# Kernel tuning notes

Measured on AMD Instinct MI355X. Metric: run time of the kernel, lower is better.

## Reference

```python
import jax, jax.numpy as jnp
import numpy as np

L, H = 6, 8          # depth, heads
DM, DH, M = 512, 64, 256  # d_model, d_head, nb random features
EPS = 1e-4


def sinusoidal_pe(n, d, dtype):
    pos = jnp.arange(n, dtype=jnp.float32)[:, None]
    div = jnp.exp(jnp.arange(0, d, 2, dtype=jnp.float32) * (-(np.log(10000.0) / d)))
    pe = jnp.zeros((n, d), jnp.float32)
    pe = pe.at[:, 0::2].set(jnp.sin(pos * div))
    pe = pe.at[:, 1::2].set(jnp.cos(pos * div))
    return pe.astype(dtype)


def layer_norm(x, g, b, eps=1e-5):
    mu = jnp.mean(x, -1, keepdims=True)
    var = jnp.mean(jnp.square(x - mu), -1, keepdims=True)
    return (x - mu) * jax.lax.rsqrt(var + eps) * g + b


def softmax_features(x, proj, is_query):
    # FAVOR+ positive softmax-kernel features. x: [b,h,n,dh], proj: [m,dh]
    dn = DH ** -0.25
    xd = x * dn
    u = jnp.einsum('bhnd,md->bhnm', xd, proj)            # [b,h,n,m]
    diag = 0.5 * jnp.sum(xd * xd, -1, keepdims=True)      # ||x||^2/2 (normalized)
    if is_query:
        stab = jnp.max(u, axis=-1, keepdims=True)
    else:
        stab = jnp.max(u, axis=(-2, -1), keepdims=True)
    return (M ** -0.5) * (jnp.exp(u - diag - stab) + EPS)


def split_heads(t, b, n):
    return t.reshape(b, n, H, DH).transpose(0, 2, 1, 3)   # [b,h,n,dh]


def reference(x, proj, ln1_g, ln1_b, wq, wk, wv, wo, bo, ln2_g, ln2_b, w1, b1, w2, b2):
    b, n, d = x.shape
    x = x + sinusoidal_pe(n, d, x.dtype)[None]
    for i in range(L):
        # --- FAVOR+ linear attention (pre-norm) ---
        h = layer_norm(x, ln1_g[i], ln1_b[i])
        q = split_heads(h @ wq[i], b, n)
        k = split_heads(h @ wk[i], b, n)
        v = split_heads(h @ wv[i], b, n)
        qp = softmax_features(q, proj[i], True)           # [b,h,n,m]
        kp = softmax_features(k, proj[i], False)
        ksum = jnp.sum(kp, axis=2)                         # [b,h,m]
        d_inv = 1.0 / jnp.einsum('bhnm,bhm->bhn', qp, ksum)
        ctx = jnp.einsum('bhnm,bhnd->bhmd', kp, v)         # [b,h,m,dh]
        o = jnp.einsum('bhnm,bhmd->bhnd', qp, ctx) * d_inv[..., None]
        o = o.transpose(0, 2, 1, 3).reshape(b, n, DM)
        x = x + o @ wo[i] + bo[i]
        # --- feed-forward (pre-norm, GELU) ---
        h = layer_norm(x, ln2_g[i], ln2_b[i])
        x = x + jax.nn.gelu(h @ w1[i] + b1[i], approximate=False) @ w2[i] + b2[i]
    return x


def setup_inputs() -> dict:
    key = jax.random.key(0)
    ks = jax.random.split(key, 9)
    s_in = DM ** -0.5
    s_ff = (4 * DM) ** -0.5
    return {
        'x':     jax.random.normal(ks[0], (8, 2048, DM), jnp.float32),
        'proj':  jax.random.normal(ks[1], (L, M, DH), jnp.float32),
        'ln1_g': jnp.ones((L, DM), jnp.float32),
        'ln1_b': jnp.zeros((L, DM), jnp.float32),
        'wq':    jax.random.normal(ks[2], (L, DM, DM), jnp.float32) * s_in,
        'wk':    jax.random.normal(ks[3], (L, DM, DM), jnp.float32) * s_in,
        'wv':    jax.random.normal(ks[4], (L, DM, DM), jnp.float32) * s_in,
        'wo':    jax.random.normal(ks[5], (L, DM, DM), jnp.float32) * s_in,
        'bo':    jnp.zeros((L, DM), jnp.float32),
        'ln2_g': jnp.ones((L, DM), jnp.float32),
        'ln2_b': jnp.zeros((L, DM), jnp.float32),
        'w1':    jax.random.normal(ks[6], (L, DM, 4 * DM), jnp.float32) * s_in,
        'b1':    jnp.zeros((L, 4 * DM), jnp.float32),
        'w2':    jax.random.normal(ks[7], (L, 4 * DM, DM), jnp.float32) * s_ff,
        'b2':    jnp.zeros((L, DM), jnp.float32),
    }
```

## Files before the change

kernel.cpp:

```cpp
#include <hip/hip_runtime.h>
#include <math.h>

#define LNUM 6
#define HNUM 8
#define DMODEL 512
#define DHEAD 64
#define MFEAT 256
#define BATCH 8
#define SEQ 2048
#define TOK (BATCH*SEQ)
#define BHN (BATCH*HNUM)
#define DFF 2048
#define EPSF 1e-4f
#define LN_EPS 1e-5f
#define DNRM 0.35355339059327373f
#define SMF 0.0625f

typedef unsigned short u16;
typedef __attribute__((ext_vector_type(8))) short bf16x8;
typedef __attribute__((ext_vector_type(4))) float f32x4;
#define MFMA16(a,b,c) __builtin_amdgcn_mfma_f32_16x16x32_bf16(a,b,c,0,0,0)

#define GLOAD16(g,l) __builtin_amdgcn_global_load_lds( \
    (const __attribute__((address_space(1))) void*)(g), \
    (__attribute__((address_space(3))) void*)(l), 16, 0, 0)

__device__ __forceinline__ u16 f2bf(float f){
  unsigned int u = __float_as_uint(f);
  u = (u + 0x7fffu + ((u >> 16) & 1u)) >> 16;
  return (u16)u;
}
__device__ __forceinline__ float bf2f(u16 s){
  return __uint_as_float(((unsigned int)s) << 16);
}
__device__ __forceinline__ void atomicMaxF(float* addr, float val){
  if(val >= 0.f) atomicMax((int*)addr, __float_as_int(val));
  else           atomicMin((unsigned int*)addr, __float_as_uint(val));
}
__device__ __forceinline__ float fast_gelu(float z){
  float g2 = z*(1.5957691216f + 0.07135481628f*z*z);
  return z / (1.0f + __expf(-g2));
}

__global__ void k_addpe(const float* __restrict__ x, float* __restrict__ xo){
  int idx = blockIdx.x*256 + threadIdx.x;
  int d = idx & (DMODEL-1);
  int n = (idx >> 9) & (SEQ-1);
  int j = d >> 1;
  float freq = expf((float)(2*j) * (-9.210340371976184f / (float)DMODEL));
  float ang = (float)n * freq;
  float pe = (d & 1) ? cosf(ang) : sinf(ang);
  xo[idx] = x[idx] + pe;
}

__global__ void k_ln(const float* __restrict__ x, const float* __restrict__ g,
                     const float* __restrict__ bv, u16* __restrict__ out){
  __shared__ float sred[8];
  int t = blockIdx.x, tid = threadIdx.x;
  const float2 v = ((const float2*)(x + (size_t)t*DMODEL))[tid];
  float s = v.x + v.y;
  #pragma unroll
  for(int o=32;o;o>>=1) s += __shfl_down(s,o);
  if((tid&63)==0) sred[tid>>6] = s;
  __syncthreads();
  if(tid==0) sred[4] = (sred[0]+sred[1]+sred[2]+sred[3]) * (1.0f/DMODEL);
  __syncthreads();
  float mu = sred[4];
  float dx = v.x - mu, dy = v.y - mu;
  float s2 = dx*dx + dy*dy;
  #pragma unroll
  for(int o=32;o;o>>=1) s2 += __shfl_down(s2,o);
  if((tid&63)==0) sred[tid>>6] = s2;
  __syncthreads();
  if(tid==0) sred[5] = rsqrtf((sred[0]+sred[1]+sred[2]+sred[3])*(1.0f/DMODEL) + LN_EPS);
  __syncthreads();
  float rs = sred[5];
  const float2 gg = ((const float2*)g)[tid];
  const float2 bb = ((const float2*)bv)[tid];
  ushort2 o2; o2.x = f2bf(dx*rs*gg.x + bb.x); o2.y = f2bf(dy*rs*gg.y + bb.y);
  ((ushort2*)(out + (size_t)t*DMODEL))[tid] = o2;
}

__global__ void k_wcvt(const float* __restrict__ w, u16* __restrict__ wt, int K, int N){
  __shared__ float sm[64][65];
  int kt = blockIdx.y*64, nt = blockIdx.x*64;
  int t = threadIdx.x;
  int c = t & 63, r4 = t >> 6;
  #pragma unroll
  for(int i=0;i<16;i++){
    int kl = i*4 + r4;
    sm[kl][c] = w[(size_t)(kt+kl)*N + nt + c];
  }
  __syncthreads();
  #pragma unroll
  for(int i=0;i<16;i++){
    int nl = i*4 + r4;
    wt[(size_t)(nt+nl)*K + kt + c] = f2bf(sm[c][nl]);
  }
}

__global__ void k_pcvt(const float* __restrict__ p, u16* __restrict__ pb){
  int i = blockIdx.x*256 + threadIdx.x;
  pb[i] = f2bf(p[i]);
}

template<int EPI>
__global__ __launch_bounds__(256,4)
void k_mm(const u16* __restrict__ A, const u16* __restrict__ Bt,
          const float* __restrict__ bias, void* __restrict__ Cv,
          int Nc, int K){
  __shared__ u16 As[2][128*32];
  __shared__ u16 Bs[2][128*32];
  int tid = threadIdx.x;
  int w = tid >> 6, lane = tid & 63;
  int wr = w >> 1, wc = w & 1;
  int hi = lane >> 4, li = lane & 15;
  int row0 = blockIdx.y*128, col0 = blockIdx.x*128;
  int lr = lane >> 2;
  int cs = (lane & 3) ^ ((lane >> 3) & 3);
  const u16* gA = A  + (size_t)(row0 + w*16 + lr)*K + cs*8;
  const u16* gB = Bt + (size_t)(col0 + w*16 + lr)*K + cs*8;
  int rb = li*32 + ((hi ^ ((li>>1)&3))<<3);
  f32x4 acc[4][4] = {};

#define STAGE_MM(b,k0) { \
    GLOAD16(gA + (k0),                &As[b][(w*16)*32]);      \
    GLOAD16(gA + (size_t)64*K + (k0), &As[b][(64+w*16)*32]);   \
    GLOAD16(gB + (k0),                &Bs[b][(w*16)*32]);      \
    GLOAD16(gB + (size_t)64*K + (k0), &Bs[b][(64+w*16)*32]); }

  int nk = K >> 5;
  STAGE_MM(0, 0)
  STAGE_MM(1, 32)
  for(int t=0; t<nk; ++t){
    __builtin_amdgcn_sched_barrier(0);
    if(t+1 < nk){ asm volatile("s_waitcnt vmcnt(4)"); }
    else        { asm volatile("s_waitcnt vmcnt(0)"); }
    __builtin_amdgcn_s_barrier();
    __builtin_amdgcn_sched_barrier(0);
    const u16* pa = &As[t&1][0];
    const u16* pb = &Bs[t&1][0];
    bf16x8 bfr[4];
    #pragma unroll
    for(int q=0;q<4;q++) bfr[q] = *(const bf16x8*)&pb[rb + wc*2048 + q*512];
    #pragma unroll
    for(int i2=0;i2<4;i2++){
      bf16x8 a = *(const bf16x8*)&pa[rb + wr*2048 + i2*512];
      #pragma unroll
      for(int j2=0;j2<4;j2++)
        acc[i2][j2] = MFMA16(a, bfr[j2], acc[i2][j2]);
    }
    __builtin_amdgcn_sched_barrier(0);
    __builtin_amdgcn_s_barrier();
    __builtin_amdgcn_sched_barrier(0);
    if(t+2 < nk){ STAGE_MM(t&1, (size_t)(t+2)*32) }
  }
#undef STAGE_MM

  #pragma unroll
  for(int i2=0;i2<4;i2++){
    #pragma unroll
    for(int j2=0;j2<4;j2++){
      int col = col0 + wc*64 + j2*16 + li;
      float bcol = (EPI==2 || EPI==3) ? bias[col] : 0.f;
      if constexpr (EPI==4){
        int nb = row0 + wr*64 + i2*16 + hi*4;
        int b = nb >> 11, n = nb & (SEQ-1);
        int h = col >> 6, dh = col & 63;
        ushort4 pk;
        pk.x = f2bf(acc[i2][j2][0]); pk.y = f2bf(acc[i2][j2][1]);
        pk.z = f2bf(acc[i2][j2][2]); pk.w = f2bf(acc[i2][j2][3]);
        *(ushort4*)((u16*)Cv + (((size_t)(b*HNUM+h)*DHEAD + dh)*SEQ + n)) = pk;
      } else {
        #pragma unroll
        for(int r=0;r<4;r++){
          int row = row0 + wr*64 + i2*16 + hi*4 + r;
          float v = acc[i2][j2][r];
          if constexpr (EPI==1){
            int b = row >> 11, n = row & (SEQ-1);
            int h = col >> 6, dh = col & 63;
            ((u16*)Cv)[((size_t)(b*HNUM+h)*SEQ + n)*DHEAD + dh] = f2bf(v);
          } else if constexpr (EPI==2){
            ((float*)Cv)[(size_t)row*Nc + col] += v + bcol;
          } else {
            ((u16*)Cv)[(size_t)row*Nc + col] = f2bf(fast_gelu(v + bcol));
          }
        }
      }
    }
  }
}

template<int PHASE>
__global__ __launch_bounds__(256)
void k_feat(const u16* __restrict__ xg, const u16* __restrict__ pjb,
            u16* __restrict__ outp, float* __restrict__ kmax,
            float* __restrict__ ksum, float* __restrict__ den){
  __shared__ u16 pj[256*64];
  __shared__ u16 xs[32*64];
  __shared__ float dgs[32];
  __shared__ float wred[4][32];
  __shared__ float wden[4][32];
  __shared__ float ksl[256];
  int tid = threadIdx.x, w = tid >> 6, lane = tid & 63;
  int hi = lane >> 4, li = lane & 15;
  int r0 = blockIdx.x * 32;
  int bh = r0 >> 11;
  #pragma unroll
  for(int i=0;i<8;i++){
    int idx = i*256 + tid;
    int m = idx >> 3, c = idx & 7;
    bf16x8 v = *(const bf16x8*)(pjb + m*64 + c*8);
    *(bf16x8*)&pj[m*64 + ((c ^ (m&7))<<3)] = v;
  }
  {
    int m = tid >> 3, c = tid & 7;
    bf16x8 v = *(const bf16x8*)(xg + (size_t)(r0+m)*64 + c*8);
    *(bf16x8*)&xs[m*64 + ((c ^ (m&7))<<3)] = v;
  }
  if constexpr (PHASE==2){ ksl[tid] = ksum[bh*MFEAT + tid]; }
  __syncthreads();
  if constexpr (PHASE!=0){
    if(tid < 32){
      float s = 0.f;
      #pragma unroll
      for(int d=0;d<64;d++){ float t = bf2f(xs[tid*64 + d]); s += t*t; }
      dgs[tid] = 0.5f*DNRM*DNRM*s;
    }
  }
  f32x4 acc[2][4] = {};
  #pragma unroll
  for(int ks=0;ks<2;ks++){
    bf16x8 af[2], bfr[4];
    int kc = ks*4 + hi;
    #pragma unroll
    for(int t=0;t<2;t++){
      int ar = t*16 + li;
      af[t] = *(const bf16x8*)&xs[ar*64 + ((kc ^ (ar&7))<<3)];
    }
    #pragma unroll
    for(int t=0;t<4;t++){
      int bc = w*64 + t*16 + li;
      bfr[t] = *(const bf16x8*)&pj[bc*64 + ((kc ^ (bc&7))<<3)];
    }
    #pragma unroll
    for(int i2=0;i2<2;i2++)
      #pragma unroll
      for(int j2=0;j2<4;j2++)
        acc[i2][j2] = MFMA16(af[i2], bfr[j2], acc[i2][j2]);
  }
  __syncthreads();
  if constexpr (PHASE==0){
    float mx = -1e30f;
    #pragma unroll
    for(int i2=0;i2<2;i2++)
      #pragma unroll
      for(int j2=0;j2<4;j2++)
        #pragma unroll
        for(int r=0;r<4;r++) mx = fmaxf(mx, acc[i2][j2][r]);
    #pragma unroll
    for(int o=32;o;o>>=1) mx = fmaxf(mx, __shfl_xor(mx,o));
    if(lane==0) wred[w][0] = mx;
    __syncthreads();
    if(tid==0){
      float m2 = fmaxf(fmaxf(wred[0][0],wred[1][0]), fmaxf(wred[2][0],wred[3][0]));
      atomicMaxF(&kmax[bh], m2*DNRM);
    }
  } else if constexpr (PHASE==1){
    float km = kmax[bh];
    float csum[4] = {0.f,0.f,0.f,0.f};
    #pragma unroll
    for(int i2=0;i2<2;i2++){
      #pragma unroll
      for(int j2=0;j2<4;j2++){
        int col = w*64 + j2*16 + li;
        ushort4 pk;
        float cpart = 0.f;
        #pragma unroll
        for(int r=0;r<4;r++){
          int rl = i2*16 + hi*4 + r;
          float u = acc[i2][j2][r]*DNRM;
          u16 eb = f2bf(SMF*(expf(u - dgs[rl] - km) + EPSF));
          ((u16*)&pk)[r] = eb;
          cpart += bf2f(eb);
        }
        *(ushort4*)(outp + ((size_t)(bh*MFEAT + col)*SEQ + (r0 & (SEQ-1)) + i2*16 + hi*4)) = pk;
        csum[j2] += cpart;
      }
    }
    #pragma unroll
    for(int j2=0;j2<4;j2++){
      float v = csum[j2];
      v += __shfl_xor(v,16); v += __shfl_xor(v,32);
      if(hi==0) atomicAdd(&ksum[bh*MFEAT + w*64 + j2*16 + li], v);
    }
  } else {
    #pragma unroll
    for(int i2=0;i2<2;i2++){
      #pragma unroll
      for(int r=0;r<4;r++){
        float v = fmaxf(fmaxf(acc[i2][0][r],acc[i2][1][r]), fmaxf(acc[i2][2][r],acc[i2][3][r]));
        v = fmaxf(v, __shfl_xor(v,1)); v = fmaxf(v, __shfl_xor(v,2));
        v = fmaxf(v, __shfl_xor(v,4)); v = fmaxf(v, __shfl_xor(v,8));
        if(li==0) wred[w][i2*16 + hi*4 + r] = v;
      }
    }
    __syncthreads();
    #pragma unroll
    for(int i2=0;i2<2;i2++){
      #pragma unroll
      for(int r=0;r<4;r++){
        int rl = i2*16 + hi*4 + r;
        float rm = fmaxf(fmaxf(wred[0][rl],wred[1][rl]), fmaxf(wred[2][rl],wred[3][rl]));
        float dsum = 0.f;
        #pragma unroll
        for(int j2=0;j2<4;j2++){
          int col = w*64 + j2*16 + li;
          float u = acc[i2][j2][r]*DNRM;
          u16 eb = f2bf(SMF*(expf(u - dgs[rl] - rm) + EPSF));
          outp[((size_t)r0 + rl)*MFEAT + col] = eb;
          dsum += bf2f(eb)*ksl[col];
        }
        dsum += __shfl_xor(dsum,1); dsum += __shfl_xor(dsum,2);
        dsum += __shfl_xor(dsum,4); dsum += __shfl_xor(dsum,8);
        if(li==0) wden[w][rl] = dsum;
      }
    }
    __syncthreads();
    if(tid < 32) den[(size_t)r0 + tid] = wden[0][tid]+wden[1][tid]+wden[2][tid]+wden[3][tid];
  }
}

__global__ __launch_bounds__(256)
void k_ctx(const u16* __restrict__ vt, const u16* __restrict__ kpt,
           u16* __restrict__ ctxt){
  __shared__ u16 As[64*64];
  __shared__ u16 Bs[64*64];
  int tid = threadIdx.x, w = tid >> 6, lane = tid & 63;
  int wr = w >> 1, wc = w & 1;
  int hi = lane >> 4, li = lane & 15;
  int bh = blockIdx.y, mb = blockIdx.x*64;
  int lr = lane >> 3;
  int lc = (lane & 7) ^ lr;
  const u16* gA = vt  + (size_t)bh*DHEAD*SEQ + (size_t)(w*8 + lr)*SEQ + lc*8;
  const u16* gB = kpt + ((size_t)bh*MFEAT + mb + w*8 + lr)*SEQ + lc*8;
  f32x4 acc[2][2] = {};
  for(int k0=0;k0<SEQ;k0+=64){
    #pragma unroll
    for(int t=0;t<2;t++){
      GLOAD16(gA + (size_t)(t*32)*SEQ + k0, &As[(t*4+w)*512]);
      GLOAD16(gB + (size_t)(t*32)*SEQ + k0, &Bs[(t*4+w)*512]);
    }
    __syncthreads();
    #pragma unroll
    for(int ks=0;ks<2;ks++){
      bf16x8 af[2], bfr[2];
      int kc = ks*4 + hi;
      #pragma unroll
      for(int t=0;t<2;t++){
        int ar = wr*32 + t*16 + li;
        af[t] = *(const bf16x8*)&As[ar*64 + ((kc ^ (ar&7))<<3)];
        int bc = wc*32 + t*16 + li;
        bfr[t] = *(const bf16x8*)&Bs[bc*64 + ((kc ^ (bc&7))<<3)];
      }
      #pragma unroll
      for(int i2=0;i2<2;i2++)
        #pragma unroll
        for(int j2=0;j2<2;j2++)
          acc[i2][j2] = MFMA16(af[i2], bfr[j2], acc[i2][j2]);
    }
    __syncthreads();
  }
  #pragma unroll
  for(int i2=0;i2<2;i2++)
    #pragma unroll
    for(int j2=0;j2<2;j2++){
      int m = mb + wc*32 + j2*16 + li;
      #pragma unroll
      for(int r=0;r<4;r++){
        int dh = wr*32 + i2*16 + hi*4 + r;
        ctxt[((size_t)bh*DHEAD + dh)*MFEAT + m] = f2bf(acc[i2][j2][r]);
      }
    }
}

__global__ __launch_bounds__(256)
void k_o(const u16* __restrict__ qp, const u16* __restrict__ ctxt,
         const float* __restrict__ den, u16* __restrict__ o){
  __shared__ u16 As[128*64];
  __shared__ u16 Bs[64*64];
  int tid = threadIdx.x, w = tid >> 6, lane = tid & 63;
  int wr = w >> 1, wc = w & 1;
  int hi = lane >> 4, li = lane & 15;
  int bh = blockIdx.y, nb = blockIdx.x*128;
  int b = bh >> 3, h = bh & 7;
  int lr = lane >> 3;
  int lc = (lane & 7) ^ lr;
  const u16* gA = qp   + ((size_t)bh*SEQ + nb + w*8 + lr)*MFEAT + lc*8;
  const u16* gB = ctxt + (size_t)bh*DHEAD*MFEAT + (size_t)(w*8 + lr)*MFEAT + lc*8;
  f32x4 acc[4][2] = {};
  for(int k0=0;k0<MFEAT;k0+=64){
    #pragma unroll
    for(int t=0;t<4;t++){
      GLOAD16(gA + (size_t)(t*32)*MFEAT + k0, &As[(t*4+w)*512]);
      if(t < 2) GLOAD16(gB + (size_t)(t*32)*MFEAT + k0, &Bs[(t*4+w)*512]);
    }
    __syncthreads();
    #pragma unroll
    for(int ks=0;ks<2;ks++){
      bf16x8 af[4], bfr[2];
      int kc = ks*4 + hi;
      #pragma unroll
      for(int t=0;t<4;t++){
        int ar = wr*64 + t*16 + li;
        af[t] = *(const bf16x8*)&As[ar*64 + ((kc ^ (ar&7))<<3)];
      }
      #pragma unroll
      for(int t=0;t<2;t++){
        int bc = wc*32 + t*16 + li;
        bfr[t] = *(const bf16x8*)&Bs[bc*64 + ((kc ^ (bc&7))<<3)];
      }
      #pragma unroll
      for(int i2=0;i2<4;i2++)
        #pragma unroll
        for(int j2=0;j2<2;j2++)
          acc[i2][j2] = MFMA16(af[i2], bfr[j2], acc[i2][j2]);
    }
    __syncthreads();
  }
  #pragma unroll
  for(int i2=0;i2<4;i2++){
    #pragma unroll
    for(int r=0;r<4;r++){
      int n = nb + wr*64 + i2*16 + hi*4 + r;
      float di = 1.0f/den[(size_t)bh*SEQ + n];
      #pragma unroll
      for(int j2=0;j2<2;j2++){
        int dh = wc*32 + j2*16 + li;
        o[((size_t)b*SEQ + n)*DMODEL + h*DHEAD + dh] = f2bf(acc[i2][j2][r]*di);
      }
    }
  }
}

__global__ void k_init(float* ksum, float* kmax){
  int i = blockIdx.x*256 + threadIdx.x;
  if(i < BHN*MFEAT) ksum[i] = 0.f;
  if(i < BHN) kmax[i] = -INFINITY;
}

extern "C" void kernel_launch(void* const* d_in, const int* in_sizes, int n_in,
                              void* d_out, int out_size, void* d_ws, size_t ws_size,
                              hipStream_t stream){
  (void)in_sizes; (void)n_in; (void)out_size; (void)ws_size;
  const float* x    = (const float*)d_in[0];
  const float* proj = (const float*)d_in[1];
  const float* ln1g = (const float*)d_in[2];
  const float* ln1b = (const float*)d_in[3];
  const float* wq   = (const float*)d_in[4];
  const float* wk   = (const float*)d_in[5];
  const float* wv   = (const float*)d_in[6];
  const float* wo   = (const float*)d_in[7];
  const float* bo   = (const float*)d_in[8];
  const float* ln2g = (const float*)d_in[9];
  const float* ln2b = (const float*)d_in[10];
  const float* w1   = (const float*)d_in[11];
  const float* b1   = (const float*)d_in[12];
  const float* w2   = (const float*)d_in[13];
  const float* b2   = (const float*)d_in[14];
  float* xo = (float*)d_out;

  char* ws = (char*)d_ws;
  u16* bufH  = (u16*)ws;  ws += (size_t)TOK*DMODEL*2;
  u16* bufA  = (u16*)ws;  ws += (size_t)TOK*DMODEL*2;
  u16* featb = (u16*)ws;  ws += (size_t)BHN*SEQ*MFEAT*2;
  u16* ctxt  = (u16*)ws;  ws += (size_t)BHN*DHEAD*MFEAT*2;
  u16* wT    = (u16*)ws;  ws += (size_t)3*1048576*2;
  u16* pjb   = (u16*)ws;  ws += (size_t)LNUM*MFEAT*DHEAD*2;
  float* ksum= (float*)ws; ws += (size_t)BHN*MFEAT*4;
  float* den = (float*)ws; ws += (size_t)BHN*SEQ*4;
  float* kmax= (float*)ws; ws += 256;

  u16* wqT = wT;
  u16* wkT = wT +  262144;
  u16* wvT = wT +  524288;
  u16* woT = wT +  786432;
  u16* w1T = wT + 1048576;
  u16* w2T = wT + 2097152;

  k_addpe<<<(TOK*DMODEL)/256, 256, 0, stream>>>(x, xo);
  k_pcvt<<<(LNUM*MFEAT*DHEAD)/256, 256, 0, stream>>>(proj, pjb);

  for(int l=0; l<LNUM; l++){
    const u16* pj_l = pjb + (size_t)l*MFEAT*DHEAD;
    k_wcvt<<<dim3(8,8),  256, 0, stream>>>(wq + (size_t)l*262144,  wqT, DMODEL, DMODEL);
    k_wcvt<<<dim3(8,8),  256, 0, stream>>>(wk + (size_t)l*262144,  wkT, DMODEL, DMODEL);
    k_wcvt<<<dim3(8,8),  256, 0, stream>>>(wv + (size_t)l*262144,  wvT, DMODEL, DMODEL);
    k_wcvt<<<dim3(8,8),  256, 0, stream>>>(wo + (size_t)l*262144,  woT, DMODEL, DMODEL);
    k_wcvt<<<dim3(32,8), 256, 0, stream>>>(w1 + (size_t)l*1048576, w1T, DMODEL, DFF);
    k_wcvt<<<dim3(8,32), 256, 0, stream>>>(w2 + (size_t)l*1048576, w2T, DFF, DMODEL);

    k_init<<<64, 256, 0, stream>>>(ksum, kmax);
    k_ln<<<TOK, 256, 0, stream>>>(xo, ln1g + l*DMODEL, ln1b + l*DMODEL, bufH);
    k_mm<1><<<dim3(4,128), 256, 0, stream>>>(bufH, wkT, nullptr, bufA, DMODEL, DMODEL);
    k_feat<0><<<(BHN*SEQ)/32, 256, 0, stream>>>(bufA, pj_l, nullptr, kmax, nullptr, nullptr);
    k_feat<1><<<(BHN*SEQ)/32, 256, 0, stream>>>(bufA, pj_l, featb, kmax, ksum, nullptr);
    k_mm<4><<<dim3(4,128), 256, 0, stream>>>(bufH, wvT, nullptr, bufA, DMODEL, DMODEL);
    k_ctx<<<dim3(4,BHN), 256, 0, stream>>>(bufA, featb, ctxt);
    k_mm<1><<<dim3(4,128), 256, 0, stream>>>(bufH, wqT, nullptr, bufA, DMODEL, DMODEL);
    k_feat<2><<<(BHN*SEQ)/32, 256, 0, stream>>>(bufA, pj_l, featb, nullptr, ksum, den);
    k_o<<<dim3(SEQ/128,BHN), 256, 0, stream>>>(featb, ctxt, den, bufH);
    k_mm<2><<<dim3(4,128), 256, 0, stream>>>(bufH, woT, bo + l*DMODEL, xo, DMODEL, DMODEL);
    k_ln<<<TOK, 256, 0, stream>>>(xo, ln2g + l*DMODEL, ln2b + l*DMODEL, bufA);
    k_mm<3><<<dim3(16,128), 256, 0, stream>>>(bufA, w1T, b1 + l*DFF, featb, DFF, DMODEL);
    k_mm<2><<<dim3(4,128), 256, 0, stream>>>(featb, w2T, b2 + l*DMODEL, xo, DMODEL, DFF);
  }
}
```

Before: 2.386 ms.

## Fuse query feature map with output contraction; double-buffer ctx; merge weight conversion launches

Query-side FAVOR+ features are now computed and kept in shared memory, then contracted directly with the per-head context matrix, which is loaded asynchronously into shared memory while the features are produced. This removes the round trip of the 32M-element query feature tensor and the denominator buffer through global memory, and drops one launch per layer. The ctx kernel gets a double-buffered global-to-LDS pipeline with manual waitcnt and barriers, and the six weight conversions plus the ksum/kmax init are merged into one launch. The fused kernel uses more shared memory per block, which can lower occupancy.

After: 2.371 ms. Within noise of the previous version (-0.6%).

```diff
diff --git a/kernel.cpp b/kernel.cpp
--- a/kernel.cpp
+++ b/kernel.cpp
@@ -81,27 +81,50 @@
   ((ushort2*)(out + (size_t)t*DMODEL))[tid] = o2;
 }
 
-__global__ void k_wcvt(const float* __restrict__ w, u16* __restrict__ wt, int K, int N){
-  __shared__ float sm[64][65];
-  int kt = blockIdx.y*64, nt = blockIdx.x*64;
-  int t = threadIdx.x;
-  int c = t & 63, r4 = t >> 6;
-  #pragma unroll
-  for(int i=0;i<16;i++){
-    int kl = i*4 + r4;
-    sm[kl][c] = w[(size_t)(kt+kl)*N + nt + c];
-  }
-  __syncthreads();
-  #pragma unroll
-  for(int i=0;i<16;i++){
-    int nl = i*4 + r4;
-    wt[(size_t)(nt+nl)*K + kt + c] = f2bf(sm[c][nl]);
-  }
-}
-
 __global__ void k_pcvt(const float* __restrict__ p, u16* __restrict__ pb){
   int i = blockIdx.x*256 + threadIdx.x;
   pb[i] = f2bf(p[i]);
+}
+
+__global__ void k_wcvt_all(const float* __restrict__ wq, const float* __restrict__ wk,
+                           const float* __restrict__ wv, const float* __restrict__ wo,
+                           const float* __restrict__ w1, const float* __restrict__ w2,
+                           u16* __restrict__ wqT, u16* __restrict__ wkT,
+                           u16* __restrict__ wvT, u16* __restrict__ woT,
+                           u16* __restrict__ w1T, u16* __restrict__ w2T,
+                           float* __restrict__ ksum, float* __restrict__ kmax){
+  int bid = blockIdx.x;
+  if(bid >= 768){
+    int i = (bid-768)*256 + threadIdx.x;
+    ksum[i] = 0.f;
+    if(i < BHN) kmax[i] = -INFINITY;
+    return;
+  }
+  const float* src; u16* dst; int K, N, bx, by;
+  if(bid < 256){
+    int which = bid >> 6, sub = bid & 63;
+    src = which==0 ? wq : which==1 ? wk : which==2 ? wv : wo;
+    dst = which==0 ? wqT : which==1 ? wkT : which==2 ? wvT : woT;
+    K = 512; N = 512; bx = sub & 7; by = sub >> 3;
+  } else if(bid < 512){
+    int sub = bid - 256; src = w1; dst = w1T; K = 512; N = 2048; bx = sub & 31; by = sub >> 5;
+  } else {
+    int sub = bid - 512; src = w2; dst = w2T; K = 2048; N = 512; bx = sub & 7; by = sub >> 3;
+  }
+  __shared__ float sm[64][65];
+  int kt = by*64, nt = bx*64;
+  int t = threadIdx.x, c = t & 63, r4 = t >> 6;
+  #pragma unroll
+  for(int i=0;i<16;i++){
+    int kl = i*4 + r4;
+    sm[kl][c] = src[(size_t)(kt+kl)*N + nt + c];
+  }
+  __syncthreads();
+  #pragma unroll
+  for(int i=0;i<16;i++){
+    int nl = i*4 + r4;
+    dst[(size_t)(nt+nl)*K + kt + c] = f2bf(sm[c][nl]);
+  }
 }
 
 template<int EPI>
@@ -195,13 +218,11 @@
 __global__ __launch_bounds__(256)
 void k_feat(const u16* __restrict__ xg, const u16* __restrict__ pjb,
             u16* __restrict__ outp, float* __restrict__ kmax,
-            float* __restrict__ ksum, float* __restrict__ den){
+            float* __restrict__ ksum){
   __shared__ u16 pj[256*64];
   __shared__ u16 xs[32*64];
   __shared__ float dgs[32];
   __shared__ float wred[4][32];
-  __shared__ float wden[4][32];
-  __shared__ float ksl[256];
   int tid = threadIdx.x, w = tid >> 6, lane = tid & 63;
   int hi = lane >> 4, li = lane & 15;
   int r0 = blockIdx.x * 32;
@@ -218,9 +239,8 @@
     bf16x8 v = *(const bf16x8*)(xg + (size_t)(r0+m)*64 + c*8);
     *(bf16x8*)&xs[m*64 + ((c ^ (m&7))<<3)] = v;
   }
-  if constexpr (PHASE==2){ ksl[tid] = ksum[bh*MFEAT + tid]; }
-  __syncthreads();
-  if constexpr (PHASE!=0){
+  __syncthreads();
+  if constexpr (PHASE==1){
     if(tid < 32){
       float s = 0.f;
       #pragma unroll
@@ -266,7 +286,7 @@
       float m2 = fmaxf(fmaxf(wred[0][0],wred[1][0]), fmaxf(wred[2][0],wred[3][0]));
       atomicMaxF(&kmax[bh], m2*DNRM);
     }
-  } else if constexpr (PHASE==1){
+  } else {
     float km = kmax[bh];
     float csum[4] = {0.f,0.f,0.f,0.f};
     #pragma unroll
@@ -294,48 +314,146 @@
       v += __shfl_xor(v,16); v += __shfl_xor(v,32);
       if(hi==0) atomicAdd(&ksum[bh*MFEAT + w*64 + j2*16 + li], v);
     }
-  } else {
-    #pragma unroll
-    for(int i2=0;i2<2;i2++){
-      #pragma unroll
-      for(int r=0;r<4;r++){
-        float v = fmaxf(fmaxf(acc[i2][0][r],acc[i2][1][r]), fmaxf(acc[i2][2][r],acc[i2][3][r]));
-        v = fmaxf(v, __shfl_xor(v,1)); v = fmaxf(v, __shfl_xor(v,2));
-        v = fmaxf(v, __shfl_xor(v,4)); v = fmaxf(v, __shfl_xor(v,8));
-        if(li==0) wred[w][i2*16 + hi*4 + r] = v;
+  }
+}
+
+__global__ __launch_bounds__(256)
+void k_feato(const u16* __restrict__ xg, const u16* __restrict__ pjb,
+             const u16* __restrict__ ctxt, const float* __restrict__ ksum,
+             u16* __restrict__ o){
+  __shared__ u16 smA[16384];
+  __shared__ u16 smX[2048];
+  __shared__ u16 smQ[8192];
+  __shared__ float dgs[32];
+  __shared__ float wred[4][32];
+  __shared__ float wden[4][32];
+  __shared__ float ksl[256];
+  __shared__ float denl[32];
+  int tid = threadIdx.x, w = tid >> 6, lane = tid & 63;
+  int hi = lane >> 4, li = lane & 15;
+  int r0 = blockIdx.x * 32;
+  int bh = r0 >> 11;
+  int b = bh >> 3, h = bh & 7;
+  #pragma unroll
+  for(int i=0;i<8;i++){
+    int idx = i*256 + tid;
+    int m = idx >> 3, c = idx & 7;
+    bf16x8 v = *(const bf16x8*)(pjb + m*64 + c*8);
+    *(bf16x8*)&smA[m*64 + ((c ^ (m&7))<<3)] = v;
+  }
+  {
+    int m = tid >> 3, c = tid & 7;
+    bf16x8 v = *(const bf16x8*)(xg + (size_t)(r0+m)*64 + c*8);
+    *(bf16x8*)&smX[m*64 + ((c ^ (m&7))<<3)] = v;
+  }
+  ksl[tid] = ksum[bh*MFEAT + tid];
+  __syncthreads();
+  if(tid < 32){
+    float s = 0.f;
+    #pragma unroll
+    for(int d=0;d<64;d++){ float t = bf2f(smX[tid*64 + d]); s += t*t; }
+    dgs[tid] = 0.5f*DNRM*DNRM*s;
+  }
+  f32x4 acc[2][4] = {};
+  #pragma unroll
+  for(int ks=0;ks<2;ks++){
+    bf16x8 af[2], bfr[4];
+    int kc = ks*4 + hi;
+    #pragma unroll
+    for(int t=0;t<2;t++){
+      int ar = t*16 + li;
+      af[t] = *(const bf16x8*)&smX[ar*64 + ((kc ^ (ar&7))<<3)];
+    }
+    #pragma unroll
+    for(int t=0;t<4;t++){
+      int bc = w*64 + t*16 + li;
+      bfr[t] = *(const bf16x8*)&smA[bc*64 + ((kc ^ (bc&7))<<3)];
+    }
+    #pragma unroll
+    for(int i2=0;i2<2;i2++)
+      #pragma unroll
+      for(int j2=0;j2<4;j2++)
+        acc[i2][j2] = MFMA16(af[i2], bfr[j2], acc[i2][j2]);
+  }
+  __syncthreads();
+  {
+    int Lc0 = w*64 + lane;
+    int row0 = Lc0 >> 5, c0 = Lc0 & 31;
+    const u16* gCl = ctxt + (size_t)bh*DHEAD*MFEAT + ((size_t)row0*32 + (c0 ^ (row0&7)))*8;
+    #pragma unroll
+    for(int i=0;i<8;i++)
+      GLOAD16(gCl + i*2048, &smA[i*2048 + w*512]);
+  }
+  #pragma unroll
+  for(int i2=0;i2<2;i2++){
+    #pragma unroll
+    for(int r=0;r<4;r++){
+      float v = fmaxf(fmaxf(acc[i2][0][r],acc[i2][1][r]), fmaxf(acc[i2][2][r],acc[i2][3][r]));
+      v = fmaxf(v, __shfl_xor(v,1)); v = fmaxf(v, __shfl_xor(v,2));
+      v = fmaxf(v, __shfl_xor(v,4)); v = fmaxf(v, __shfl_xor(v,8));
+      if(li==0) wred[w][i2*16 + hi*4 + r] = v;
+    }
+  }
+  __builtin_amdgcn_sched_barrier(0);
+  asm volatile("s_waitcnt lgkmcnt(0)");
+  __builtin_amdgcn_s_barrier();
+  __builtin_amdgcn_sched_barrier(0);
+  #pragma unroll
+  for(int i2=0;i2<2;i2++){
+    #pragma unroll
+    for(int r=0;r<4;r++){
+      int rl = i2*16 + hi*4 + r;
+      float rm = fmaxf(fmaxf(wred[0][rl],wred[1][rl]), fmaxf(wred[2][rl],wred[3][rl]));
+      float dsum = 0.f;
+      #pragma unroll
+      for(int j2=0;j2<4;j2++){
+        int col = w*64 + j2*16 + li;
+        float u = acc[i2][j2][r]*DNRM;
+        u16 eb = f2bf(SMF*(expf(u - dgs[rl] - rm) + EPSF));
+        smQ[rl*256 + (((col>>3) ^ (rl&7))<<3) + (col&7)] = eb;
+        dsum += bf2f(eb)*ksl[col];
       }
-    }
-    __syncthreads();
-    #pragma unroll
-    for(int i2=0;i2<2;i2++){
-      #pragma unroll
-      for(int r=0;r<4;r++){
-        int rl = i2*16 + hi*4 + r;
-        float rm = fmaxf(fmaxf(wred[0][rl],wred[1][rl]), fmaxf(wred[2][rl],wred[3][rl]));
-        float dsum = 0.f;
-        #pragma unroll
-        for(int j2=0;j2<4;j2++){
-          int col = w*64 + j2*16 + li;
-          float u = acc[i2][j2][r]*DNRM;
-          u16 eb = f2bf(SMF*(expf(u - dgs[rl] - rm) + EPSF));
-          outp[((size_t)r0 + rl)*MFEAT + col] = eb;
-          dsum += bf2f(eb)*ksl[col];
-        }
-        dsum += __shfl_xor(dsum,1); dsum += __shfl_xor(dsum,2);
-        dsum += __shfl_xor(dsum,4); dsum += __shfl_xor(dsum,8);
-        if(li==0) wden[w][rl] = dsum;
-      }
-    }
-    __syncthreads();
-    if(tid < 32) den[(size_t)r0 + tid] = wden[0][tid]+wden[1][tid]+wden[2][tid]+wden[3][tid];
+      dsum += __shfl_xor(dsum,1); dsum += __shfl_xor(dsum,2);
+      dsum += __shfl_xor(dsum,4); dsum += __shfl_xor(dsum,8);
+      if(li==0) wden[w][rl] = dsum;
+    }
+  }
+  __builtin_amdgcn_sched_barrier(0);
+  asm volatile("s_waitcnt vmcnt(0) lgkmcnt(0)");
+  __builtin_amdgcn_s_barrier();
+  __builtin_amdgcn_sched_barrier(0);
+  if(tid < 32) denl[tid] = wden[0][tid]+wden[1][tid]+wden[2][tid]+wden[3][tid];
+  f32x4 acc2[2] = {};
+  #pragma unroll
+  for(int s=0;s<8;s++){
+    int kc = s*4 + hi;
+    int bc = w*16 + li;
+    bf16x8 bf = *(const bf16x8*)&smA[bc*256 + ((kc ^ (bc&7))<<3)];
+    #pragma unroll
+    for(int t=0;t<2;t++){
+      int ar = t*16 + li;
+      bf16x8 aa = *(const bf16x8*)&smQ[ar*256 + ((kc ^ (ar&7))<<3)];
+      acc2[t] = MFMA16(aa, bf, acc2[t]);
+    }
+  }
+  __syncthreads();
+  int nbase = r0 & (SEQ-1);
+  #pragma unroll
+  for(int t=0;t<2;t++){
+    #pragma unroll
+    for(int r=0;r<4;r++){
+      int nl = t*16 + hi*4 + r;
+      float di = 1.0f/denl[nl];
+      o[((size_t)b*SEQ + nbase + nl)*DMODEL + h*DHEAD + w*16 + li] = f2bf(acc2[t][r]*di);
+    }
   }
 }
 
 __global__ __launch_bounds__(256)
 void k_ctx(const u16* __restrict__ vt, const u16* __restrict__ kpt,
            u16* __restrict__ ctxt){
-  __shared__ u16 As[64*64];
-  __shared__ u16 Bs[64*64];
+  __shared__ u16 As[2][64*64];
+  __shared__ u16 Bs[2][64*64];
   int tid = threadIdx.x, w = tid >> 6, lane = tid & 63;
   int wr = w >> 1, wc = w & 1;
   int hi = lane >> 4, li = lane & 15;
@@ -345,23 +463,32 @@
   const u16* gA = vt  + (size_t)bh*DHEAD*SEQ + (size_t)(w*8 + lr)*SEQ + lc*8;
   const u16* gB = kpt + ((size_t)bh*MFEAT + mb + w*8 + lr)*SEQ + lc*8;
   f32x4 acc[2][2] = {};
-  for(int k0=0;k0<SEQ;k0+=64){
-    #pragma unroll
-    for(int t=0;t<2;t++){
-      GLOAD16(gA + (size_t)(t*32)*SEQ + k0, &As[(t*4+w)*512]);
-      GLOAD16(gB + (size_t)(t*32)*SEQ + k0, &Bs[(t*4+w)*512]);
-    }
-    __syncthreads();
+#define STAGE_CTX(b,k0) { \
+    GLOAD16(gA + (k0),                 &As[b][(w*8)*64]);      \
+    GLOAD16(gA + (size_t)32*SEQ + (k0),&As[b][(32+w*8)*64]);   \
+    GLOAD16(gB + (k0),                 &Bs[b][(w*8)*64]);      \
+    GLOAD16(gB + (size_t)32*SEQ + (k0),&Bs[b][(32+w*8)*64]); }
+  int nk = SEQ/64;
+  STAGE_CTX(0, 0)
+  STAGE_CTX(1, 64)
+  for(int t=0; t<nk; ++t){
+    __builtin_amdgcn_sched_barrier(0);
+    if(t+1 < nk){ asm volatile("s_waitcnt vmcnt(4)"); }
+    else        { asm volatile("s_waitcnt vmcnt(0)"); }
+    __builtin_amdgcn_s_barrier();
+    __builtin_amdgcn_sched_barrier(0);
+    const u16* pa = &As[t&1][0];
+    const u16* pb = &Bs[t&1][0];
     #pragma unroll
     for(int ks=0;ks<2;ks++){
       bf16x8 af[2], bfr[2];
       int kc = ks*4 + hi;
       #pragma unroll
-      for(int t=0;t<2;t++){
-        int ar = wr*32 + t*16 + li;
-        af[t] = *(const bf16x8*)&As[ar*64 + ((kc ^ (ar&7))<<3)];
-        int bc = wc*32 + t*16 + li;
-        bfr[t] = *(const bf16x8*)&Bs[bc*64 + ((kc ^ (bc&7))<<3)];
+      for(int q=0;q<2;q++){
+        int ar = wr*32 + q*16 + li;
+        af[q] = *(const bf16x8*)&pa[ar*64 + ((kc ^ (ar&7))<<3)];
+        int bc = wc*32 + q*16 + li;
+        bfr[q] = *(const bf16x8*)&pb[bc*64 + ((kc ^ (bc&7))<<3)];
       }
       #pragma unroll
       for(int i2=0;i2<2;i2++)
@@ -369,8 +496,12 @@
         for(int j2=0;j2<2;j2++)
           acc[i2][j2] = MFMA16(af[i2], bfr[j2], acc[i2][j2]);
     }
-    __syncthreads();
-  }
+    __builtin_amdgcn_sched_barrier(0);
+    __builtin_amdgcn_s_barrier();
+    __builtin_amdgcn_sched_barrier(0);
+    if(t+2 < nk){ STAGE_CTX(t&1, (size_t)(t+2)*64) }
+  }
+#undef STAGE_CTX
   #pragma unroll
   for(int i2=0;i2<2;i2++)
     #pragma unroll
@@ -382,71 +513,6 @@
         ctxt[((size_t)bh*DHEAD + dh)*MFEAT + m] = f2bf(acc[i2][j2][r]);
       }
     }
-}
-
-__global__ __launch_bounds__(256)
-void k_o(const u16* __restrict__ qp, const u16* __restrict__ ctxt,
-         const float* __restrict__ den, u16* __restrict__ o){
-  __shared__ u16 As[128*64];
-  __shared__ u16 Bs[64*64];
-  int tid = threadIdx.x, w = tid >> 6, lane = tid & 63;
-  int wr = w >> 1, wc = w & 1;
-  int hi = lane >> 4, li = lane & 15;
-  int bh = blockIdx.y, nb = blockIdx.x*128;
-  int b = bh >> 3, h = bh & 7;
-  int lr = lane >> 3;
-  int lc = (lane & 7) ^ lr;
-  const u16* gA = qp   + ((size_t)bh*SEQ + nb + w*8 + lr)*MFEAT + lc*8;
-  const u16* gB = ctxt + (size_t)bh*DHEAD*MFEAT + (size_t)(w*8 + lr)*MFEAT + lc*8;
-  f32x4 acc[4][2] = {};
-  for(int k0=0;k0<MFEAT;k0+=64){
-    #pragma unroll
-    for(int t=0;t<4;t++){
-      GLOAD16(gA + (size_t)(t*32)*MFEAT + k0, &As[(t*4+w)*512]);
-      if(t < 2) GLOAD16(gB + (size_t)(t*32)*MFEAT + k0, &Bs[(t*4+w)*512]);
-    }
-    __syncthreads();
-    #pragma unroll
-    for(int ks=0;ks<2;ks++){
-      bf16x8 af[4], bfr[2];
-      int kc = ks*4 + hi;
-      #pragma unroll
-      for(int t=0;t<4;t++){
-        int ar = wr*64 + t*16 + li;
-        af[t] = *(const bf16x8*)&As[ar*64 + ((kc ^ (ar&7))<<3)];
-      }
-      #pragma unroll
-      for(int t=0;t<2;t++){
-        int bc = wc*32 + t*16 + li;
-        bfr[t] = *(const bf16x8*)&Bs[bc*64 + ((kc ^ (bc&7))<<3)];
-      }
-      #pragma unroll
-      for(int i2=0;i2<4;i2++)
-        #pragma unroll
-        for(int j2=0;j2<2;j2++)
-          acc[i2][j2] = MFMA16(af[i2], bfr[j2], acc[i2][j2]);
-    }
-    __syncthreads();
-  }
-  #pragma unroll
-  for(int i2=0;i2<4;i2++){
-    #pragma unroll
-    for(int r=0;r<4;r++){
-      int n = nb + wr*64 + i2*16 + hi*4 + r;
-      float di = 1.0f/den[(size_t)bh*SEQ + n];
-      #pragma unroll
-      for(int j2=0;j2<2;j2++){
-        int dh = wc*32 + j2*16 + li;
-        o[((size_t)b*SEQ + n)*DMODEL + h*DHEAD + dh] = f2bf(acc[i2][j2][r]*di);
-      }
-    }
-  }
-}
-
-__global__ void k_init(float* ksum, float* kmax){
-  int i = blockIdx.x*256 + threadIdx.x;
-  if(i < BHN*MFEAT) ksum[i] = 0.f;
-  if(i < BHN) kmax[i] = -INFINITY;
 }
 
 extern "C" void kernel_launch(void* const* d_in, const int* in_sizes, int n_in,
@@ -478,7 +544,7 @@
   u16* wT    = (u16*)ws;  ws += (size_t)3*1048576*2;
   u16* pjb   = (u16*)ws;  ws += (size_t)LNUM*MFEAT*DHEAD*2;
   float* ksum= (float*)ws; ws += (size_t)BHN*MFEAT*4;
-  float* den = (float*)ws; ws += (size_t)BHN*SEQ*4;
+  float* den = (float*)ws; ws += (size_t)BHN*SEQ*4;  (void)den;
   float* kmax= (float*)ws; ws += 256;
 
   u16* wqT = wT;
@@ -493,23 +559,18 @@
 
   for(int l=0; l<LNUM; l++){
     const u16* pj_l = pjb + (size_t)l*MFEAT*DHEAD;
-    k_wcvt<<<dim3(8,8),  256, 0, stream>>>(wq + (size_t)l*262144,  wqT, DMODEL, DMODEL);
-    k_wcvt<<<dim3(8,8),  256, 0, stream>>>(wk + (size_t)l*262144,  wkT, DMODEL, DMODEL);
-    k_wcvt<<<dim3(8,8),  256, 0, stream>>>(wv + (size_t)l*262144,  wvT, DMODEL, DMODEL);
-    k_wcvt<<<dim3(8,8),  256, 0, stream>>>(wo + (size_t)l*262144,  woT, DMODEL, DMODEL);
-    k_wcvt<<<dim3(32,8), 256, 0, stream>>>(w1 + (size_t)l*1048576, w1T, DMODEL, DFF);
-    k_wcvt<<<dim3(8,32), 256, 0, stream>>>(w2 + (size_t)l*1048576, w2T, DFF, DMODEL);
-
-    k_init<<<64, 256, 0, stream>>>(ksum, kmax);
+    k_wcvt_all<<<832, 256, 0, stream>>>(wq + (size_t)l*262144, wk + (size_t)l*262144,
+                                        wv + (size_t)l*262144, wo + (size_t)l*262144,
+                                        w1 + (size_t)l*1048576, w2 + (size_t)l*1048576,
+                                        wqT, wkT, wvT, woT, w1T, w2T, ksum, kmax);
     k_ln<<<TOK, 256, 0, stream>>>(xo, ln1g + l*DMODEL, ln1b + l*DMODEL, bufH);
     k_mm<1><<<dim3(4,128), 256, 0, stream>>>(bufH, wkT, nullptr, bufA, DMODEL, DMODEL);
-    k_feat<0><<<(BHN*SEQ)/32, 256, 0, stream>>>(bufA, pj_l, nullptr, kmax, nullptr, nullptr);
-    k_feat<1><<<(BHN*SEQ)/32, 256, 0, stream>>>(bufA, pj_l, featb, kmax, ksum, nullptr);
+    k_feat<0><<<(BHN*SEQ)/32, 256, 0, stream>>>(bufA, pj_l, nullptr, kmax, nullptr);
+    k_feat<1><<<(BHN*SEQ)/32, 256, 0, stream>>>(bufA, pj_l, featb, kmax, ksum);
     k_mm<4><<<dim3(4,128), 256, 0, stream>>>(bufH, wvT, nullptr, bufA, DMODEL, DMODEL);
     k_ctx<<<dim3(4,BHN), 256, 0, stream>>>(bufA, featb, ctxt);
     k_mm<1><<<dim3(4,128), 256, 0, stream>>>(bufH, wqT, nullptr, bufA, DMODEL, DMODEL);
-    k_feat<2><<<(BHN*SEQ)/32, 256, 0, stream>>>(bufA, pj_l, featb, nullptr, ksum, den);
-    k_o<<<dim3(SEQ/128,BHN), 256, 0, stream>>>(featb, ctxt, den, bufH);
+    k_feato<<<(BHN*SEQ)/32, 256, 0, stream>>>(bufA, pj_l, ctxt, ksum, bufH);
     k_mm<2><<<dim3(4,128), 256, 0, stream>>>(bufH, woT, bo + l*DMODEL, xo, DMODEL, DMODEL);
     k_ln<<<TOK, 256, 0, stream>>>(xo, ln2g + l*DMODEL, ln2b + l*DMODEL, bufA);
     k_mm<3><<<dim3(16,128), 256, 0, stream>>>(bufA, w1T, b1 + l*DFF, featb, DFF, DMODEL);
```
